# Kernel tuning notes

Measured on AMD Instinct MI355X. Metric: run time of the kernel, lower is better.

Reference implementation:

```python
import jax, jax.numpy as jnp
from jax import lax
import numpy as np

TWO_PI = 2.0 * np.pi

# ---- batched real-amplitude statevector simulator (RY/CNOT only -> real state) ----

def _init_state(batch, n):
    s = jnp.zeros((batch, 2 ** n), dtype=jnp.float32).at[:, 0].set(1.0)
    return s.reshape((batch,) + (2,) * n)

def _ry(state, wire, theta, n):
    # state: (B, 2,...,2); theta: scalar or (B,)
    ax = wire + 1
    h = theta * 0.5
    c = jnp.reshape(jnp.cos(h), (-1,) + (1,) * (n - 1))
    s = jnp.reshape(jnp.sin(h), (-1,) + (1,) * (n - 1))
    s0 = lax.index_in_dim(state, 0, ax, keepdims=False)
    s1 = lax.index_in_dim(state, 1, ax, keepdims=False)
    return jnp.stack([c * s0 - s * s1, s * s0 + c * s1], axis=ax)

def _cnot(state, ctrl, tgt):
    axc, axt = ctrl + 1, tgt + 1
    s0 = lax.index_in_dim(state, 0, axc, keepdims=True)
    s1 = lax.index_in_dim(state, 1, axc, keepdims=True)
    return jnp.concatenate([s0, jnp.flip(s1, axis=axt)], axis=axc)

def _expz(state, wire, n):
    sgn = jnp.reshape(jnp.array([1.0, -1.0], state.dtype),
                      (1,) * (wire + 1) + (2,) + (1,) * (n - wire - 1))
    return jnp.sum(state * state * sgn, axis=tuple(range(1, n + 1)))

# gate lists: ('ry', theta_index, wire) or ('cx', control, target)
EDGE_OPS = [('ry',0,0),('ry',1,1),('cx',0,1),('ry',2,2),('ry',3,3),('cx',3,2),
            ('ry',4,4),('ry',5,5),('cx',4,5),('ry',6,6),('ry',7,7),('cx',7,6),
            ('ry',8,1),('ry',9,2),('cx',1,2),('ry',10,5),('ry',11,6),('cx',6,5),
            ('ry',12,2),('ry',13,5),('cx',2,5),('ry',14,5)]

NODE_OPS = [('ry',0,0),('ry',1,1),('cx',0,1),('ry',2,2),('ry',3,3),('cx',3,2),
            ('ry',4,4),('ry',5,5),('cx',4,5),('ry',6,6),('ry',7,7),('cx',7,6),
            ('ry',8,8),('ry',9,9),('cx',8,9),('ry',10,10),('ry',11,11),('cx',11,10),
            ('ry',12,1),('ry',13,2),('cx',1,2),('ry',14,5),('ry',15,6),('cx',6,5),
            ('ry',16,9),('ry',17,10),('cx',10,9),('ry',18,2),('ry',19,5),('cx',2,5),
            ('ry',20,5),('ry',21,9),('cx',5,9),('ry',22,4)]

def _circuit(angles, theta, ops, n, meas_wire):
    st = _init_state(angles.shape[0], n)
    for i in range(n):  # input encoding RYs, per-sample angles
        st = _ry(st, i, angles[:, i], n)
    for op in ops:
        if op[0] == 'ry':
            st = _ry(st, op[2], theta[op[1]], n)
        else:
            st = _cnot(st, op[1], op[2])
    return _expz(st, meas_wire, n)

# ---- GNN pieces ----

def _edge_net(H, Ri, Ro, theta):
    bo = Ro.T @ H                      # [E,4]
    bi = Ri.T @ H                      # [E,4]
    B = jnp.concatenate([bo, bi], axis=1)  # [E,8]
    return (1.0 - _circuit(B, theta, EDGE_OPS, 8, 5)) * 0.5

def _node_net(H, e, Ri, Ro, theta):
    bo = Ro.T @ H                      # [E,4]
    bi = Ri.T @ H                      # [E,4]
    mi = (Ri * e[None, :]) @ bo        # [N,4]
    mo = (Ro * e[None, :]) @ bi        # [N,4]
    M = jnp.concatenate([mi, mo, H], axis=1)  # [N,12]
    return jnp.pi * (1.0 - _circuit(M, theta, NODE_OPS, 12, 9))

def _gnn(X, Ri, Ro, W_in, b_in, theta_edge, theta_node, n_iters=2):
    H = jnp.concatenate([jax.nn.sigmoid(X @ W_in + b_in) * TWO_PI, X], axis=1)  # [N,4]
    e = _edge_net(H, Ri, Ro, theta_edge)
    for _ in range(n_iters):
        h = _node_net(H, e, Ri, Ro, theta_node)   # [N]
        H = jnp.concatenate([h[:, None], X], axis=1)
        e = _edge_net(H, Ri, Ro, theta_edge)
    return e


def setup_inputs() -> dict:
    key = jax.random.key(0)
    ks = jax.random.split(key, 6)
    N, E = 2048, 4096
    X = jax.random.normal(ks[0], (N, 3), jnp.float32)
    recv = jax.random.randint(ks[1], (E,), 0, N)
    send = jax.random.randint(ks[2], (E,), 0, N)
    cols = jnp.arange(E)
    Ri = jnp.zeros((N, E), jnp.float32).at[recv, cols].set(1.0)
    Ro = jnp.zeros((N, E), jnp.float32).at[send, cols].set(1.0)
    W_in = jax.random.normal(ks[3], (3, 1), jnp.float32)
    b_in = jnp.zeros((1,), jnp.float32)
    theta_edge = jax.random.uniform(ks[4], (15,), jnp.float32, 0.0, TWO_PI)
    theta_node = jax.random.uniform(ks[5], (23,), jnp.float32, 0.0, TWO_PI)
    return {'X': X, 'Ri': Ri, 'Ro': Ro, 'W_in': W_in, 'b_in': b_in,
            'theta_edge': theta_edge, 'theta_node': theta_node}


def reference(X, Ri, Ro, W_in, b_in, theta_edge, theta_node):
    return _gnn(X, Ri, Ro, W_in, b_in, theta_edge, theta_node, n_iters=2)
```

## Files before the change

kernel.cpp:

```cpp
#include <hip/hip_runtime.h>
#include <math.h>

#define N_NODES 2048
#define N_EDGES 4096
#define PI_F 3.14159265358979323846f
#define TWO_PI_F 6.28318530717958647692f

template<int M>
__device__ __forceinline__ float shflx(float v) {
    if constexpr (M == 1) {
        return __int_as_float(__builtin_amdgcn_mov_dpp(
            __float_as_int(v), 0xB1, 0xF, 0xF, false));
    } else if constexpr (M == 2) {
        return __int_as_float(__builtin_amdgcn_mov_dpp(
            __float_as_int(v), 0x4E, 0xF, 0xF, false));
    } else if constexpr (M == 8) {
        return __int_as_float(__builtin_amdgcn_mov_dpp(
            __float_as_int(v), 0x128, 0xF, 0xF, false));
    } else {
        return __shfl_xor(v, M, 64);
    }
}

__device__ __forceinline__ float wave_sum(float p) {
    p += shflx<32>(p); p += shflx<16>(p); p += shflx<8>(p);
    p += shflx<4>(p);  p += shflx<2>(p);  p += shflx<1>(p);
    return p;
}


template<int NA, int B>
__device__ __forceinline__ void ry_j(float* a, float c, float s) {
#pragma unroll
    for (int j = 0; j < NA; ++j) {
        if ((j & (1 << B)) == 0) {
            int k = j | (1 << B);
            float x0 = a[j], x1 = a[k];
            a[j] = c * x0 - s * x1;
            a[k] = s * x0 + c * x1;
        }
    }
}

template<int NA, int MASK>
__device__ __forceinline__ void ry_l(float* a, float c, float s, int lane) {
    float ss = (lane & MASK) ? s : -s;
#pragma unroll
    for (int j = 0; j < NA; ++j) {
        float p = shflx<MASK>(a[j]);
        a[j] = c * a[j] + ss * p;
    }
}

template<int NA, int BC, int BT>
__device__ __forceinline__ void cx_jj(float* a) {
#pragma unroll
    for (int j = 0; j < NA; ++j) {
        if ((j & (1 << BC)) && !(j & (1 << BT))) {
            int k = j | (1 << BT);
            float t = a[j]; a[j] = a[k]; a[k] = t;
        }
    }
}

template<int NA, int MC, int BT>
__device__ __forceinline__ void cx_lj(float* a, int lane) {
    bool sel = (lane & MC) != 0;
#pragma unroll
    for (int j = 0; j < NA; ++j) {
        if ((j & (1 << BT)) == 0) {
            int k = j | (1 << BT);
            float t0 = a[j], t1 = a[k];
            a[j] = sel ? t1 : t0;
            a[k] = sel ? t0 : t1;
        }
    }
}

template<int NA, int MC, int MT>
__device__ __forceinline__ void cx_ll(float* a, int lane) {
    bool sel = (lane & MC) != 0;
#pragma unroll
    for (int j = 0; j < NA; ++j) {
        float p = shflx<MT>(a[j]);
        a[j] = sel ? p : a[j];
    }
}

__global__ __launch_bounds__(256) void k_setup(
        const float* __restrict__ X, const float* __restrict__ Ri,
        const float* __restrict__ Ro, const float* __restrict__ W,
        const float* __restrict__ b, const float* __restrict__ te,
        const float* __restrict__ tn,
        int* __restrict__ send, int* __restrict__ recv, float* __restrict__ H,
        float* __restrict__ htrig,
        float* __restrict__ maccA, float* __restrict__ maccB,
        float* __restrict__ trig) {
    int tid = blockIdx.x * blockDim.x + threadIdx.x;
    if (tid < N_NODES) {
        float x0 = X[tid*3+0], x1 = X[tid*3+1], x2 = X[tid*3+2];
        float z = x0*W[0] + x1*W[1] + x2*W[2] + b[0];
        float sg = 1.0f / (1.0f + __expf(-z));
        float h = sg * TWO_PI_F;
        H[tid*4+0] = h;
        H[tid*4+1] = x0; H[tid*4+2] = x1; H[tid*4+3] = x2;
        float c0,s0,c1,s1,c2,s2,c3,s3;
        __sincosf(0.5f*h,  &s0, &c0);
        __sincosf(0.5f*x0, &s1, &c1);
        __sincosf(0.5f*x1, &s2, &c2);
        __sincosf(0.5f*x2, &s3, &c3);
        ((float4*)htrig)[tid*2+0] = make_float4(c0, s0, c1, s1);
        ((float4*)htrig)[tid*2+1] = make_float4(c2, s2, c3, s3);
    }
    if (tid < N_NODES * 8) { maccA[tid] = 0.f; maccB[tid] = 0.f; }
    if (tid >= 4096 && tid < 4096 + 15) {
        int i = tid - 4096; float s, c;
        __sincosf(0.5f * te[i], &s, &c);
        trig[i] = c; trig[16 + i] = s;
    }
    if (tid >= 4224 && tid < 4224 + 23) {
        int i = tid - 4224; float s, c;
        __sincosf(0.5f * tn[i], &s, &c);
        trig[32 + i] = c; trig[56 + i] = s;
    }
    const float4 vi = ((const float4*)Ri)[tid];
    const float4 vo = ((const float4*)Ro)[tid];
    int base = tid * 4;
    int n = base >> 12;
    int e = base & (N_EDGES - 1);
    if (vi.x != 0.f) recv[e+0] = n;
    if (vi.y != 0.f) recv[e+1] = n;
    if (vi.z != 0.f) recv[e+2] = n;
    if (vi.w != 0.f) recv[e+3] = n;
    if (vo.x != 0.f) send[e+0] = n;
    if (vo.y != 0.f) send[e+1] = n;
    if (vo.z != 0.f) send[e+2] = n;
    if (vo.w != 0.f) send[e+3] = n;
}

template<bool SCATTER>
__global__ __launch_bounds__(256) void k_edge(
        const float* __restrict__ H, const float* __restrict__ htrig,
        const int* __restrict__ send, const int* __restrict__ recv,
        const float* __restrict__ trig,
        float* __restrict__ out, float* __restrict__ macc) {
    int e = (blockIdx.x * blockDim.x + threadIdx.x) >> 6;
    int lane = threadIdx.x & 63;
    int si = send[e], ri = recv[e];
    float4 t0 = ((const float4*)htrig)[si*2+0];
    float4 t1 = ((const float4*)htrig)[si*2+1];
    float4 t2 = ((const float4*)htrig)[ri*2+0];
    float4 t3 = ((const float4*)htrig)[ri*2+1];
    float ec[8] = {t0.x, t0.z, t1.x, t1.z, t2.x, t2.z, t3.x, t3.z};
    float es[8] = {t0.y, t0.w, t1.y, t1.w, t2.y, t2.w, t3.y, t3.w};

    float lp;
    {
        float f0 = (lane&32) ? es[0] : ec[0];
        float f1 = (lane&16) ? es[1] : ec[1];
        float f3 = (lane& 8) ? es[3] : ec[3];
        float f4 = (lane& 4) ? es[4] : ec[4];
        float f6 = (lane& 2) ? es[6] : ec[6];
        float f7 = (lane& 1) ? es[7] : ec[7];
        lp = f0*f1*f3*f4*f6*f7;
    }
    float a[4];
    a[0] = lp;
    a[1] = a[0]*es[5]; a[0] *= ec[5];
    a[2] = a[0]*es[2]; a[3] = a[1]*es[2];
    a[0] *= ec[2];     a[1] *= ec[2];

    const float* tc = trig;
    const float* ts = trig + 16;

    ry_l<4,32>(a, tc[0], ts[0], lane);
    ry_l<4,16>(a, tc[1], ts[1], lane);
    cx_ll<4,32,16>(a, lane);
    ry_j<4,1>(a, tc[2], ts[2]);
    ry_l<4,8>(a, tc[3], ts[3], lane);
    cx_lj<4,8,1>(a, lane);
    ry_l<4,4>(a, tc[4], ts[4], lane);
    ry_j<4,0>(a, tc[5], ts[5]);
    cx_lj<4,4,0>(a, lane);
    ry_l<4,2>(a, tc[6], ts[6], lane);
    ry_l<4,1>(a, tc[7], ts[7], lane);
    cx_ll<4,1,2>(a, lane);
    ry_l<4,16>(a, tc[8], ts[8], lane);
    ry_j<4,1>(a, tc[9], ts[9]);
    cx_lj<4,16,1>(a, lane);
    ry_j<4,0>(a, tc[10], ts[10]);
    ry_l<4,2>(a, tc[11], ts[11], lane);
    cx_lj<4,2,0>(a, lane);
    ry_j<4,1>(a, tc[12], ts[12]);
    ry_j<4,0>(a, tc[13], ts[13]);
    cx_jj<4,1,0>(a);
    ry_j<4,0>(a, tc[14], ts[14]);

    float p = (a[0]*a[0] + a[2]*a[2]) - (a[1]*a[1] + a[3]*a[3]);
    p = wave_sum(p);
    float ev = (1.0f - p) * 0.5f;

    if (SCATTER) {
        if (lane < 8) {
            float4 hs = ((const float4*)H)[si];
            float4 hr = ((const float4*)H)[ri];
            float B[8] = {hs.x, hs.y, hs.z, hs.w, hr.x, hr.y, hr.z, hr.w};
            float bv = B[0];
            if (lane == 1) bv = B[1]; if (lane == 2) bv = B[2]; if (lane == 3) bv = B[3];
            if (lane == 4) bv = B[4]; if (lane == 5) bv = B[5]; if (lane == 6) bv = B[6];
            if (lane == 7) bv = B[7];
            int idx = (lane < 4) ? (ri*8 + lane) : (si*8 + 4 + (lane & 3));
            atomicAdd(&macc[idx], ev * bv);
        }
    } else {
        if (lane == 0) out[e] = ev;
    }
}

__global__ __launch_bounds__(256) void k_node(
        const float* __restrict__ macc, float* __restrict__ H,
        float* __restrict__ htrig, const float* __restrict__ trig) {
    __shared__ float part[2][2];
    int wb   = threadIdx.x >> 6;
    int lane = threadIdx.x & 63;
    int pair = wb >> 1;
    int par  = wb & 1;
    int n = blockIdx.x * 2 + pair;

    float4 m0 = ((const float4*)macc)[n*2];
    float4 m1 = ((const float4*)macc)[n*2+1];
    float M[8] = {m0.x, m0.y, m0.z, m0.w, m1.x, m1.y, m1.z, m1.w};

    float mc[12], ms[12];
#pragma unroll
    for (int k = 0; k < 8; ++k) __sincosf(0.5f * M[k], &ms[k], &mc[k]);
    {
        float4 t0 = ((const float4*)htrig)[n*2+0];
        float4 t1 = ((const float4*)htrig)[n*2+1];
        mc[8] = t0.x; ms[8] = t0.y; mc[9]  = t0.z; ms[9]  = t0.w;
        mc[10]= t1.x; ms[10]= t1.y; mc[11] = t1.z; ms[11] = t1.w;
    }

    float lp;
    {
        float f0 = (lane&32) ? ms[0] : mc[0];
        float f1 = (lane&16) ? ms[1] : mc[1];
        float f3 = (lane& 8) ? ms[3] : mc[3];
        float f4 = (lane& 4) ? ms[4] : mc[4];
        float f7 = (lane& 2) ? ms[7] : mc[7];
        float f8 = (lane& 1) ? ms[8] : mc[8];
        lp = f0*f1*f3*f4*f7*f8;
    }
    float a[32];
    a[0] = lp;
    {
        const int jw[5] = {10, 9, 6, 5, 2};
#pragma unroll
        for (int bnum = 0; bnum < 5; ++bnum) {
            int sz = 1 << bnum;
            float cw = mc[jw[bnum]], sw = ms[jw[bnum]];
#pragma unroll
            for (int k = 0; k < 32; ++k) {
                if (k < sz) {
                    a[k + sz] = a[k] * sw;
                    a[k] *= cw;
                }
            }
        }
    }

    const float* tc = trig + 32;
    const float* ts = trig + 56;

    ry_l<32,32>(a, tc[0], ts[0], lane);
    ry_l<32,16>(a, tc[1], ts[1], lane);
    cx_ll<32,32,16>(a, lane);
    ry_j<32,4>(a, tc[2], ts[2]);
    ry_l<32,8>(a, tc[3], ts[3], lane);
    cx_lj<32,8,4>(a, lane);
    ry_l<32,4>(a, tc[4], ts[4], lane);
    ry_j<32,3>(a, tc[5], ts[5]);
    cx_lj<32,4,3>(a, lane);
    ry_j<32,2>(a, tc[6], ts[6]);
    ry_l<32,2>(a, tc[7], ts[7], lane);
    cx_lj<32,2,2>(a, lane);
    ry_l<32,1>(a, tc[8], ts[8], lane);
    ry_j<32,1>(a, tc[9], ts[9]);
    cx_lj<32,1,1>(a, lane);
    ry_j<32,0>(a, tc[10], ts[10]);
    {
        float f = par ? (ts[11]*mc[11] + tc[11]*ms[11])
                      : (tc[11]*mc[11] - ts[11]*ms[11]);
#pragma unroll
        for (int j = 0; j < 32; ++j) a[j] *= f;
    }
    if (par) {
#pragma unroll
        for (int j = 0; j < 32; j += 2) {
            float t = a[j]; a[j] = a[j+1]; a[j+1] = t;
        }
    }
    ry_l<32,16>(a, tc[12], ts[12], lane);
    ry_j<32,4>(a, tc[13], ts[13]);
    cx_lj<32,16,4>(a, lane);
    ry_j<32,3>(a, tc[14], ts[14]);
    ry_j<32,2>(a, tc[15], ts[15]);
    cx_jj<32,2,3>(a);
    ry_j<32,1>(a, tc[16], ts[16]);
    ry_j<32,0>(a, tc[17], ts[17]);
    cx_jj<32,0,1>(a);
    ry_j<32,4>(a, tc[18], ts[18]);
    ry_j<32,3>(a, tc[19], ts[19]);
    cx_jj<32,4,3>(a);
    ry_j<32,3>(a, tc[20], ts[20]);
    ry_j<32,1>(a, tc[21], ts[21]);
    cx_jj<32,3,1>(a);

    float p = 0.f;
#pragma unroll
    for (int j = 0; j < 32; ++j) {
        float q = a[j]*a[j];
        p += (j & 2) ? -q : q;
    }
    p = wave_sum(p);
    if (lane == 0) part[pair][par] = p;
    __syncthreads();
    if (lane == 0 && par == 0) {
        float h = PI_F * (1.0f - (part[pair][0] + part[pair][1]));
        H[n*4+0] = h;
        float sh, ch;
        __sincosf(0.5f * h, &sh, &ch);
        htrig[n*8+0] = ch;
        htrig[n*8+1] = sh;
    }
}

extern "C" void kernel_launch(void* const* d_in, const int* in_sizes, int n_in,
                              void* d_out, int out_size, void* d_ws, size_t ws_size,
                              hipStream_t stream) {
    const float* X  = (const float*)d_in[0];
    const float* Ri = (const float*)d_in[1];
    const float* Ro = (const float*)d_in[2];
    const float* W  = (const float*)d_in[3];
    const float* b  = (const float*)d_in[4];
    const float* te = (const float*)d_in[5];
    const float* tn = (const float*)d_in[6];
    float* out = (float*)d_out;

    int*   send  = (int*)d_ws;
    int*   recv  = send + N_EDGES;
    float* H     = (float*)(recv + N_EDGES);
    float* htrig = H + N_NODES * 4;
    float* ebuf  = htrig + N_NODES * 8;
    float* maccA = ebuf + N_EDGES;
    float* maccB = maccA + N_NODES * 8;
    float* trig  = maccB + N_NODES * 8;

    int total4 = (N_NODES * N_EDGES) / 4;
    k_setup<<<total4 / 256, 256, 0, stream>>>(X, Ri, Ro, W, b, te, tn,
                                              send, recv, H, htrig,
                                              maccA, maccB, trig);
    k_edge<true ><<<N_EDGES / 4, 256, 0, stream>>>(H, htrig, send, recv, trig, ebuf, maccA);
    k_node<<<N_NODES / 2, 256, 0, stream>>>(maccA, H, htrig, trig);
    k_edge<true ><<<N_EDGES / 4, 256, 0, stream>>>(H, htrig, send, recv, trig, ebuf, maccB);
    k_node<<<N_NODES / 2, 256, 0, stream>>>(maccB, H, htrig, trig);
    k_edge<false><<<N_EDGES / 4, 256, 0, stream>>>(H, htrig, send, recv, trig, out, nullptr);
}
```

Baseline: 147.1 us.

## Fuse edge/node phases into one persistent kernel with grid barriers

```diff
diff --git a/kernel.cpp b/kernel.cpp
--- a/kernel.cpp
+++ b/kernel.cpp
@@ -3,6 +3,7 @@
 
 #define N_NODES 2048
 #define N_EDGES 4096
+#define NBLK 256
 #define PI_F 3.14159265358979323846f
 #define TWO_PI_F 6.28318530717958647692f
 
@@ -87,6 +88,20 @@
     }
 }
 
+__device__ __forceinline__ void gridbar(int* cell) {
+    __syncthreads();
+    if (threadIdx.x == 0) {
+        __threadfence();
+        __hip_atomic_fetch_add(cell, 1, __ATOMIC_RELAXED,
+                               __HIP_MEMORY_SCOPE_AGENT);
+        while (__hip_atomic_load(cell, __ATOMIC_RELAXED,
+                                 __HIP_MEMORY_SCOPE_AGENT) < NBLK)
+            __builtin_amdgcn_s_sleep(1);
+        __threadfence();
+    }
+    __syncthreads();
+}
+
 __global__ __launch_bounds__(256) void k_setup(
         const float* __restrict__ X, const float* __restrict__ Ri,
         const float* __restrict__ Ro, const float* __restrict__ W,
@@ -95,7 +110,7 @@
         int* __restrict__ send, int* __restrict__ recv, float* __restrict__ H,
         float* __restrict__ htrig,
         float* __restrict__ maccA, float* __restrict__ maccB,
-        float* __restrict__ trig) {
+        float* __restrict__ trig, int* __restrict__ bar) {
     int tid = blockIdx.x * blockDim.x + threadIdx.x;
     if (tid < N_NODES) {
         float x0 = X[tid*3+0], x1 = X[tid*3+1], x2 = X[tid*3+2];
@@ -113,6 +128,7 @@
         ((float4*)htrig)[tid*2+1] = make_float4(c2, s2, c3, s3);
     }
     if (tid < N_NODES * 8) { maccA[tid] = 0.f; maccB[tid] = 0.f; }
+    if (tid < 4) bar[tid] = 0;
     if (tid >= 4096 && tid < 4096 + 15) {
         int i = tid - 4096; float s, c;
         __sincosf(0.5f * te[i], &s, &c);
@@ -139,13 +155,12 @@
 }
 
 template<bool SCATTER>
-__global__ __launch_bounds__(256) void k_edge(
+__device__ __forceinline__ void edge_phase(
+        int e, int lane,
         const float* __restrict__ H, const float* __restrict__ htrig,
         const int* __restrict__ send, const int* __restrict__ recv,
         const float* __restrict__ trig,
         float* __restrict__ out, float* __restrict__ macc) {
-    int e = (blockIdx.x * blockDim.x + threadIdx.x) >> 6;
-    int lane = threadIdx.x & 63;
     int si = send[e], ri = recv[e];
     float4 t0 = ((const float4*)htrig)[si*2+0];
     float4 t1 = ((const float4*)htrig)[si*2+1];
@@ -217,16 +232,11 @@
     }
 }
 
-__global__ __launch_bounds__(256) void k_node(
+__device__ __forceinline__ void node_phase(
+        int n, int par, int pair, int lane,
         const float* __restrict__ macc, float* __restrict__ H,
-        float* __restrict__ htrig, const float* __restrict__ trig) {
-    __shared__ float part[2][2];
-    int wb   = threadIdx.x >> 6;
-    int lane = threadIdx.x & 63;
-    int pair = wb >> 1;
-    int par  = wb & 1;
-    int n = blockIdx.x * 2 + pair;
-
+        float* __restrict__ htrig, const float* __restrict__ trig,
+        float part[8][2]) {
     float4 m0 = ((const float4*)macc)[n*2];
     float4 m1 = ((const float4*)macc)[n*2+1];
     float M[8] = {m0.x, m0.y, m0.z, m0.w, m1.x, m1.y, m1.z, m1.w};
@@ -335,6 +345,31 @@
     }
 }
 
+__global__ __launch_bounds__(1024, 4) void k_mega(
+        float* __restrict__ H, float* __restrict__ htrig,
+        const int* __restrict__ send, const int* __restrict__ recv,
+        const float* __restrict__ trig,
+        float* __restrict__ maccA, float* __restrict__ maccB,
+        float* __restrict__ out, int* __restrict__ bar) {
+    __shared__ float part[8][2];
+    int w    = threadIdx.x >> 6;
+    int lane = threadIdx.x & 63;
+    int e    = blockIdx.x * 16 + w;
+    int n    = blockIdx.x * 8 + (w >> 1);
+    int par  = w & 1;
+    int pair = w >> 1;
+
+    edge_phase<true >(e, lane, H, htrig, send, recv, trig, nullptr, maccA);
+    gridbar(&bar[0]);
+    node_phase(n, par, pair, lane, maccA, H, htrig, trig, part);
+    gridbar(&bar[1]);
+    edge_phase<true >(e, lane, H, htrig, send, recv, trig, nullptr, maccB);
+    gridbar(&bar[2]);
+    node_phase(n, par, pair, lane, maccB, H, htrig, trig, part);
+    gridbar(&bar[3]);
+    edge_phase<false>(e, lane, H, htrig, send, recv, trig, out, nullptr);
+}
+
 extern "C" void kernel_launch(void* const* d_in, const int* in_sizes, int n_in,
                               void* d_out, int out_size, void* d_ws, size_t ws_size,
                               hipStream_t stream) {
@@ -351,18 +386,15 @@
     int*   recv  = send + N_EDGES;
     float* H     = (float*)(recv + N_EDGES);
     float* htrig = H + N_NODES * 4;
-    float* ebuf  = htrig + N_NODES * 8;
-    float* maccA = ebuf + N_EDGES;
+    float* maccA = htrig + N_NODES * 8;
     float* maccB = maccA + N_NODES * 8;
     float* trig  = maccB + N_NODES * 8;
+    int*   bar   = (int*)(trig + 128);
 
     int total4 = (N_NODES * N_EDGES) / 4;
     k_setup<<<total4 / 256, 256, 0, stream>>>(X, Ri, Ro, W, b, te, tn,
                                               send, recv, H, htrig,
-                                              maccA, maccB, trig);
-    k_edge<true ><<<N_EDGES / 4, 256, 0, stream>>>(H, htrig, send, recv, trig, ebuf, maccA);
-    k_node<<<N_NODES / 2, 256, 0, stream>>>(maccA, H, htrig, trig);
-    k_edge<true ><<<N_EDGES / 4, 256, 0, stream>>>(H, htrig, send, recv, trig, ebuf, maccB);
-    k_node<<<N_NODES / 2, 256, 0, stream>>>(maccB, H, htrig, trig);
-    k_edge<false><<<N_EDGES / 4, 256, 0, stream>>>(H, htrig, send, recv, trig, out, nullptr);
-}
+                                              maccA, maccB, trig, bar);
+    k_mega<<<NBLK, 1024, 0, stream>>>(H, htrig, send, recv, trig,
+                                      maccA, maccB, out, bar);
+}
```

Measured after the change: 199.0 us. 35.3% more time.
